# Performance work log

Hardware: AMD Instinct MI355X
Metric: run time of the kernel (lower is better)

The kernel has to match this reference:

```python
import jax, jax.numpy as jnp
import numpy as np
import math

B, S, D = 4, 2048, 1024

def setup_inputs() -> dict:
    key = jax.random.key(0)
    k_x, k_q, k_k, k_v = jax.random.split(key, 4)
    scale = 1.0 / math.sqrt(D)
    return {
        "x": jax.random.normal(k_x, (B, S, D), dtype=jnp.float32),
        "W_Q": jax.random.normal(k_q, (D, D), dtype=jnp.float32) * scale,
        "W_K": jax.random.normal(k_k, (D, D), dtype=jnp.float32) * scale,
        "W_V": jax.random.normal(k_v, (D, D), dtype=jnp.float32) * scale,
    }

def reference(x, W_Q, W_K, W_V):
    # nn.Linear(bias=False): y = x @ W.T
    Q = jnp.einsum('bsd,ed->bse', x, W_Q)
    K = jnp.einsum('bsd,ed->bse', x, W_K)
    V = jnp.einsum('bsd,ed->bse', x, W_V)
    scores = jnp.einsum('bqd,bkd->bqk', Q, K) / jnp.sqrt(jnp.asarray(Q.shape[-1], Q.dtype))
    weight = jax.nn.softmax(scores, axis=-1)  # [B,S,S]
    return jnp.einsum('bqk,bkd->bqd', weight, V)
```

## Files before the change

kernel.cpp:

```cpp
#include <hip/hip_runtime.h>
#include <stdint.h>

typedef __bf16 bf16;
typedef __bf16 bf16x8 __attribute__((ext_vector_type(8)));
typedef __bf16 bf16x4 __attribute__((ext_vector_type(4)));
typedef float f32x4 __attribute__((ext_vector_type(4)));

__device__ inline void gload_lds16(const void* g, void* l) {
  __builtin_amdgcn_global_load_lds(
      (__attribute__((address_space(1))) void*)g,
      (__attribute__((address_space(3))) void*)l, 16, 0, 0);
}

__global__ __launch_bounds__(256) void cvt_f32_bf16(const float* __restrict__ in,
                                                    bf16* __restrict__ out, int n4) {
  int i = blockIdx.x * blockDim.x + threadIdx.x;
  int stride = gridDim.x * blockDim.x;
  for (; i < n4; i += stride) {
    float4 v = ((const float4*)in)[i];
    bf16x4 o;
    o[0] = (bf16)v.x; o[1] = (bf16)v.y; o[2] = (bf16)v.z; o[3] = (bf16)v.w;
    ((bf16x4*)out)[i] = o;
  }
}

template <int MODE, int BN>
__global__ __launch_bounds__(512, 2) void gemm8(
    const bf16* __restrict__ Ag, const bf16* __restrict__ Bg,
    void* __restrict__ Cg, void* __restrict__ C2g,
    long lda, long ldb, long ldc,
    long sA, long sB, long sC, int K, float scale)
{
  constexpr int BUFSZ = 32768 + BN * 128;
  constexpr int MACC = (BN == 256) ? 8 : 4;
  __shared__ alignas(16) char lds[2 * BUFSZ];
  const int tid = threadIdx.x;
  const int l = tid & 63;
  const int wv = tid >> 6;
  const int fr = l & 15;
  const int kch = l >> 4;
  const int m0 = blockIdx.y * 256;
  const int n0 = blockIdx.x * BN;
  const bf16* Ab = Ag + (long)blockIdx.z * sA;
  const bf16* Bb = Bg + (long)blockIdx.z * sB;

  const int wm = (BN == 256) ? (wv >> 2) : (wv >> 1);
  const int wn = (BN == 256) ? (wv & 3) : (wv & 1);

  int a_rd, b_rd;
  if constexpr (BN == 256) {
    a_rd = fr * 128 + (((wm * 4 + kch) ^ (fr & 7)) << 4);
    b_rd = (wn & 1) * 8192 + fr * 128 + ((((wn >> 1) * 4 + kch) ^ (fr & 7)) << 4);
  } else {
    a_rd = (wm & 1) * 8192 + fr * 128 + ((((wm >> 1) * 4 + kch) ^ (fr & 7)) << 4);
    b_rd = fr * 128 + (((wn * 4 + kch) ^ (fr & 7)) << 4);
  }

  const int se = (tid & 7) ^ ((tid >> 3) & 7);
  const int s_rowA = (se >> 2) * 128 + (tid >> 3);
  const int s_rowB = (BN == 256) ? s_rowA : ((se >> 2) * 64 + (tid >> 3));
  const int s_k = (se & 3) * 8;
  const int wb16 = (tid & 448) * 16;

  const int NT = K >> 6;
  f32x4 acc[MACC][4] = {};

  auto stageA = [&](int tile, int kh, int buf) {
#pragma unroll
    for (int rd = 0; rd < 2; ++rd)
      gload_lds16(Ab + (long)(m0 + s_rowA + rd * 64) * lda + tile * 64 + kh * 32 + s_k,
                  lds + buf * BUFSZ + kh * 16384 + rd * 8192 + wb16);
  };
  auto stageB = [&](int tile, int kh, int buf) {
    if constexpr (BN == 256) {
#pragma unroll
      for (int rd = 0; rd < 2; ++rd)
        gload_lds16(Bb + (long)(n0 + s_rowB + rd * 64) * ldb + tile * 64 + kh * 32 + s_k,
                    lds + buf * BUFSZ + 32768 + kh * 16384 + rd * 8192 + wb16);
    } else {
      gload_lds16(Bb + (long)(n0 + s_rowB) * ldb + tile * 64 + kh * 32 + s_k,
                  lds + buf * BUFSZ + 32768 + kh * 8192 + wb16);
    }
  };

  stageA(0, 0, 0); stageB(0, 0, 0); stageA(0, 1, 0); stageB(0, 1, 0);
  stageA(min(1, NT - 1), 0, 1); stageB(min(1, NT - 1), 0, 1);
  if constexpr (BN == 256) asm volatile("s_waitcnt vmcnt(4)" ::: "memory");
  else                     asm volatile("s_waitcnt vmcnt(3)" ::: "memory");
  __builtin_amdgcn_sched_barrier(0);
  __builtin_amdgcn_s_barrier();

  for (int t = 0; t < NT; ++t) {
    const char* bufA = lds + (t & 1) * BUFSZ;
    const char* bufB = bufA + 32768;
    const int t1 = min(t + 1, NT - 1);
    const int t2 = min(t + 2, NT - 1);
    const int nb = (t & 1) ^ 1;
    const int cur = t & 1;

    if constexpr (BN == 256) {
      bf16x8 bfg[4], af[4];
      stageA(t1, 1, nb);
#pragma unroll
      for (int n = 0; n < 4; ++n) bfg[n] = *(const bf16x8*)(bufB + n * 2048 + b_rd);
#pragma unroll
      for (int m = 0; m < 4; ++m) af[m] = *(const bf16x8*)(bufA + m * 2048 + a_rd);
      __builtin_amdgcn_s_barrier();
      __builtin_amdgcn_s_setprio(1);
#pragma unroll
      for (int m = 0; m < 4; ++m)
#pragma unroll
        for (int n = 0; n < 4; ++n)
          acc[m][n] = __builtin_amdgcn_mfma_f32_16x16x32_bf16(af[m], bfg[n], acc[m][n], 0, 0, 0);
      __builtin_amdgcn_s_setprio(0);
      __builtin_amdgcn_s_barrier();
      stageB(t1, 1, nb);
#pragma unroll
      for (int m = 0; m < 4; ++m) af[m] = *(const bf16x8*)(bufA + 8192 + m * 2048 + a_rd);
      __builtin_amdgcn_s_barrier();
      __builtin_amdgcn_s_setprio(1);
#pragma unroll
      for (int m = 0; m < 4; ++m)
#pragma unroll
        for (int n = 0; n < 4; ++n)
          acc[4 + m][n] = __builtin_amdgcn_mfma_f32_16x16x32_bf16(af[m], bfg[n], acc[4 + m][n], 0, 0, 0);
      __builtin_amdgcn_s_setprio(0);
      __builtin_amdgcn_s_barrier();
      stageA(t2, 0, cur);
#pragma unroll
      for (int n = 0; n < 4; ++n) bfg[n] = *(const bf16x8*)(bufB + 16384 + n * 2048 + b_rd);
#pragma unroll
      for (int m = 0; m < 4; ++m) af[m] = *(const bf16x8*)(bufA + 16384 + m * 2048 + a_rd);
      __builtin_amdgcn_s_barrier();
      __builtin_amdgcn_s_setprio(1);
#pragma unroll
      for (int m = 0; m < 4; ++m)
#pragma unroll
        for (int n = 0; n < 4; ++n)
          acc[m][n] = __builtin_amdgcn_mfma_f32_16x16x32_bf16(af[m], bfg[n], acc[m][n], 0, 0, 0);
      __builtin_amdgcn_s_setprio(0);
      __builtin_amdgcn_s_barrier();
      stageB(t2, 0, cur);
#pragma unroll
      for (int m = 0; m < 4; ++m) af[m] = *(const bf16x8*)(bufA + 16384 + 8192 + m * 2048 + a_rd);
      __builtin_amdgcn_s_barrier();
      __builtin_amdgcn_s_setprio(1);
#pragma unroll
      for (int m = 0; m < 4; ++m)
#pragma unroll
        for (int n = 0; n < 4; ++n)
          acc[4 + m][n] = __builtin_amdgcn_mfma_f32_16x16x32_bf16(af[m], bfg[n], acc[4 + m][n], 0, 0, 0);
      __builtin_amdgcn_s_setprio(0);
      asm volatile("s_waitcnt vmcnt(4)" ::: "memory");
      __builtin_amdgcn_sched_barrier(0);
      __builtin_amdgcn_s_barrier();
    } else {
      bf16x8 bfg[4], af[4];
      stageA(t1, 1, nb); stageB(t1, 1, nb);
#pragma unroll
      for (int n = 0; n < 4; ++n) bfg[n] = *(const bf16x8*)(bufB + n * 2048 + b_rd);
#pragma unroll
      for (int m = 0; m < 4; ++m) af[m] = *(const bf16x8*)(bufA + m * 2048 + a_rd);
      __builtin_amdgcn_s_barrier();
      __builtin_amdgcn_s_setprio(1);
#pragma unroll
      for (int m = 0; m < 4; ++m)
#pragma unroll
        for (int n = 0; n < 4; ++n)
          acc[m][n] = __builtin_amdgcn_mfma_f32_16x16x32_bf16(af[m], bfg[n], acc[m][n], 0, 0, 0);
      __builtin_amdgcn_s_setprio(0);
      __builtin_amdgcn_s_barrier();
      stageA(t2, 0, cur); stageB(t2, 0, cur);
#pragma unroll
      for (int n = 0; n < 4; ++n) bfg[n] = *(const bf16x8*)(bufB + 8192 + n * 2048 + b_rd);
#pragma unroll
      for (int m = 0; m < 4; ++m) af[m] = *(const bf16x8*)(bufA + 16384 + m * 2048 + a_rd);
      __builtin_amdgcn_s_barrier();
      __builtin_amdgcn_s_setprio(1);
#pragma unroll
      for (int m = 0; m < 4; ++m)
#pragma unroll
        for (int n = 0; n < 4; ++n)
          acc[m][n] = __builtin_amdgcn_mfma_f32_16x16x32_bf16(af[m], bfg[n], acc[m][n], 0, 0, 0);
      __builtin_amdgcn_s_setprio(0);
      asm volatile("s_waitcnt vmcnt(3)" ::: "memory");
      __builtin_amdgcn_sched_barrier(0);
      __builtin_amdgcn_s_barrier();
    }
  }
  asm volatile("s_waitcnt vmcnt(0)" ::: "memory");

#pragma unroll
  for (int mf = 0; mf < MACC; ++mf) {
    int row;
    if constexpr (BN == 256)
      row = m0 + wm * 128 + (mf >> 2) * 64 + (mf & 3) * 16 + (l >> 4) * 4;
    else
      row = m0 + wm * 64 + mf * 16 + (l >> 4) * 4;
#pragma unroll
    for (int n = 0; n < 4; ++n) {
      const int col = n0 + wn * 64 + n * 16 + fr;
      if constexpr (MODE == 0) {
        if (col < 2048) {
          bf16* C = (bf16*)Cg;
#pragma unroll
          for (int r = 0; r < 4; ++r)
            C[(long)(row + r) * 2048 + col] = (bf16)acc[mf][n][r];
        } else {
          bf16* Vt = (bf16*)C2g;
          const int d = col - 2048;
          const int b = row >> 11;
          const int s = row & 2047;
          bf16x4 pk;
#pragma unroll
          for (int r = 0; r < 4; ++r) pk[r] = (bf16)acc[mf][n][r];
          *(bf16x4*)(Vt + (long)b * 2097152 + (long)d * 2048 + s) = pk;
        }
      } else if constexpr (MODE == 1) {
        float* C = (float*)Cg + (long)blockIdx.z * sC;
#pragma unroll
        for (int r = 0; r < 4; ++r)
          C[(long)(row + r) * ldc + col] = acc[mf][n][r] * scale;
      } else {
        bf16* C = (bf16*)Cg + (long)blockIdx.z * sC;
#pragma unroll
        for (int r = 0; r < 4; ++r)
          C[(long)(row + r) * ldc + col] = (bf16)(acc[mf][n][r] * scale);
      }
    }
  }
}

__global__ __launch_bounds__(256) void softmax_k(const bf16* __restrict__ Sm,
                                                 bf16* __restrict__ P, int cols) {
  __shared__ float red[8];
  const long row = blockIdx.x;
  const bf16* sr = Sm + row * (long)cols;
  bf16* pr = P + row * (long)cols;
  const int t = threadIdx.x;
  bf16x8 v = *(const bf16x8*)(sr + t * 8);
  float e[8];
#pragma unroll
  for (int j = 0; j < 8; ++j) e[j] = (float)v[j];
  float m = e[0];
#pragma unroll
  for (int j = 1; j < 8; ++j) m = fmaxf(m, e[j]);
#pragma unroll
  for (int o = 32; o; o >>= 1) m = fmaxf(m, __shfl_xor(m, o));
  if ((t & 63) == 0) red[t >> 6] = m;
  __syncthreads();
  m = fmaxf(fmaxf(red[0], red[1]), fmaxf(red[2], red[3]));
  float s = 0.f;
#pragma unroll
  for (int j = 0; j < 8; ++j) { e[j] = __expf(e[j] - m); s += e[j]; }
#pragma unroll
  for (int o = 32; o; o >>= 1) s += __shfl_xor(s, o);
  if ((t & 63) == 0) red[4 + (t >> 6)] = s;
  __syncthreads();
  s = red[4] + red[5] + red[6] + red[7];
  const float inv = 1.0f / s;
  bf16x8 o8;
#pragma unroll
  for (int j = 0; j < 8; ++j) o8[j] = (bf16)(e[j] * inv);
  *(bf16x8*)(pr + t * 8) = o8;
}

extern "C" void kernel_launch(void* const* d_in, const int* in_sizes, int n_in,
                              void* d_out, int out_size, void* d_ws, size_t ws_size,
                              hipStream_t stream) {
  const float* x  = (const float*)d_in[0];
  const float* Wq = (const float*)d_in[1];
  const float* Wk = (const float*)d_in[2];
  const float* Wv = (const float*)d_in[3];
  float* out = (float*)d_out;

  const int D = 1024;

  char* ws = (char*)d_ws;
  bf16* QKbuf = (bf16*)(ws);
  bf16* P     = (bf16*)(ws);
  bf16* Vt    = (bf16*)(ws + 33554432);
  bf16* scb   = (bf16*)(ws + 50331648);
  bf16* xb    = (bf16*)(ws + 50331648);
  bf16* Wb    = (bf16*)(ws + 67108864);

  dim3 b256(256, 1, 1), b512(512, 1, 1);

  cvt_f32_bf16<<<2048, b256, 0, stream>>>(x, xb, 8192 * 1024 / 4);
  cvt_f32_bf16<<<512, b256, 0, stream>>>(Wq, Wb,             D * D / 4);
  cvt_f32_bf16<<<512, b256, 0, stream>>>(Wk, Wb + 1048576,   D * D / 4);
  cvt_f32_bf16<<<512, b256, 0, stream>>>(Wv, Wb + 2097152,   D * D / 4);

  gemm8<0, 128><<<dim3(24, 32, 1), b512, 0, stream>>>(
      xb, Wb, QKbuf, Vt, 1024, 1024, 2048, 0, 0, 0, 1024, 1.f);

  gemm8<2, 256><<<dim3(8, 8, 4), b512, 0, stream>>>(
      QKbuf, QKbuf + 1024, scb, nullptr, 2048, 2048, 2048,
      4194304, 4194304, 4194304, 1024, 0.03125f);

  softmax_k<<<8192, b256, 0, stream>>>(scb, P, 2048);

  gemm8<1, 128><<<dim3(8, 8, 4), b512, 0, stream>>>(
      P, Vt, out, nullptr, 2048, 2048, 1024,
      4194304, 2097152, 2097152, 2048, 1.f);
}
```

Before: 183.7 us.

## Fuse conversion kernels and use 128x128 GEMM tiles for projection and PV

The four f32-to-bf16 conversion launches become one combined kernel, which cuts launch overhead. A new 256-thread GEMM with 128x128 tiles replaces the 256x128 512-thread variant for the QKV projection and the P·V product. This doubles the grid size (1536 and 512 blocks) for better CU occupancy and load balance on the 256-CU device, at the cost of lower per-block data reuse. The 256x256 gemm8 is kept only for the QK^T scores.

```diff
diff --git a/kernel.cpp b/kernel.cpp
--- a/kernel.cpp
+++ b/kernel.cpp
@@ -12,27 +12,37 @@
       (__attribute__((address_space(3))) void*)l, 16, 0, 0);
 }
 
-__global__ __launch_bounds__(256) void cvt_f32_bf16(const float* __restrict__ in,
-                                                    bf16* __restrict__ out, int n4) {
-  int i = blockIdx.x * blockDim.x + threadIdx.x;
-  int stride = gridDim.x * blockDim.x;
-  for (; i < n4; i += stride) {
-    float4 v = ((const float4*)in)[i];
+__global__ __launch_bounds__(256) void cvt_all(
+    const float* __restrict__ x, const float* __restrict__ wq,
+    const float* __restrict__ wk, const float* __restrict__ wv,
+    bf16* __restrict__ xb, bf16* __restrict__ Wb) {
+  const int NX = 2097152;
+  const int NW = 262144;
+  int i = blockIdx.x * 256 + threadIdx.x;
+  const int stride = gridDim.x * 256;
+  for (int p = i; p < NX + 3 * NW; p += stride) {
+    const float* src; bf16* dst; int off;
+    if (p < NX) { src = x; dst = xb; off = p; }
+    else {
+      int q = p - NX; int w = q >> 18; off = q & (NW - 1);
+      src = (w == 0) ? wq : ((w == 1) ? wk : wv);
+      dst = Wb + (long)w * 1048576;
+    }
+    float4 v = ((const float4*)src)[off];
     bf16x4 o;
     o[0] = (bf16)v.x; o[1] = (bf16)v.y; o[2] = (bf16)v.z; o[3] = (bf16)v.w;
-    ((bf16x4*)out)[i] = o;
-  }
-}
-
-template <int MODE, int BN>
+    ((bf16x4*)dst)[off] = o;
+  }
+}
+
+template <int MODE>
 __global__ __launch_bounds__(512, 2) void gemm8(
     const bf16* __restrict__ Ag, const bf16* __restrict__ Bg,
-    void* __restrict__ Cg, void* __restrict__ C2g,
+    void* __restrict__ Cg,
     long lda, long ldb, long ldc,
     long sA, long sB, long sC, int K, float scale)
 {
-  constexpr int BUFSZ = 32768 + BN * 128;
-  constexpr int MACC = (BN == 256) ? 8 : 4;
+  constexpr int BUFSZ = 65536;
   __shared__ alignas(16) char lds[2 * BUFSZ];
   const int tid = threadIdx.x;
   const int l = tid & 63;
@@ -40,53 +50,40 @@
   const int fr = l & 15;
   const int kch = l >> 4;
   const int m0 = blockIdx.y * 256;
-  const int n0 = blockIdx.x * BN;
+  const int n0 = blockIdx.x * 256;
   const bf16* Ab = Ag + (long)blockIdx.z * sA;
   const bf16* Bb = Bg + (long)blockIdx.z * sB;
 
-  const int wm = (BN == 256) ? (wv >> 2) : (wv >> 1);
-  const int wn = (BN == 256) ? (wv & 3) : (wv & 1);
-
-  int a_rd, b_rd;
-  if constexpr (BN == 256) {
-    a_rd = fr * 128 + (((wm * 4 + kch) ^ (fr & 7)) << 4);
-    b_rd = (wn & 1) * 8192 + fr * 128 + ((((wn >> 1) * 4 + kch) ^ (fr & 7)) << 4);
-  } else {
-    a_rd = (wm & 1) * 8192 + fr * 128 + ((((wm >> 1) * 4 + kch) ^ (fr & 7)) << 4);
-    b_rd = fr * 128 + (((wn * 4 + kch) ^ (fr & 7)) << 4);
-  }
+  const int wm = wv >> 2;
+  const int wn = wv & 3;
+
+  const int a_rd = fr * 128 + (((wm * 4 + kch) ^ (fr & 7)) << 4);
+  const int b_rd = (wn & 1) * 8192 + fr * 128 + ((((wn >> 1) * 4 + kch) ^ (fr & 7)) << 4);
 
   const int se = (tid & 7) ^ ((tid >> 3) & 7);
-  const int s_rowA = (se >> 2) * 128 + (tid >> 3);
-  const int s_rowB = (BN == 256) ? s_rowA : ((se >> 2) * 64 + (tid >> 3));
+  const int s_row = (se >> 2) * 128 + (tid >> 3);
   const int s_k = (se & 3) * 8;
   const int wb16 = (tid & 448) * 16;
 
   const int NT = K >> 6;
-  f32x4 acc[MACC][4] = {};
+  f32x4 acc[8][4] = {};
 
   auto stageA = [&](int tile, int kh, int buf) {
 #pragma unroll
     for (int rd = 0; rd < 2; ++rd)
-      gload_lds16(Ab + (long)(m0 + s_rowA + rd * 64) * lda + tile * 64 + kh * 32 + s_k,
+      gload_lds16(Ab + (long)(m0 + s_row + rd * 64) * lda + tile * 64 + kh * 32 + s_k,
                   lds + buf * BUFSZ + kh * 16384 + rd * 8192 + wb16);
   };
   auto stageB = [&](int tile, int kh, int buf) {
-    if constexpr (BN == 256) {
-#pragma unroll
-      for (int rd = 0; rd < 2; ++rd)
-        gload_lds16(Bb + (long)(n0 + s_rowB + rd * 64) * ldb + tile * 64 + kh * 32 + s_k,
-                    lds + buf * BUFSZ + 32768 + kh * 16384 + rd * 8192 + wb16);
-    } else {
-      gload_lds16(Bb + (long)(n0 + s_rowB) * ldb + tile * 64 + kh * 32 + s_k,
-                  lds + buf * BUFSZ + 32768 + kh * 8192 + wb16);
-    }
+#pragma unroll
+    for (int rd = 0; rd < 2; ++rd)
+      gload_lds16(Bb + (long)(n0 + s_row + rd * 64) * ldb + tile * 64 + kh * 32 + s_k,
+                  lds + buf * BUFSZ + 32768 + kh * 16384 + rd * 8192 + wb16);
   };
 
   stageA(0, 0, 0); stageB(0, 0, 0); stageA(0, 1, 0); stageB(0, 1, 0);
   stageA(min(1, NT - 1), 0, 1); stageB(min(1, NT - 1), 0, 1);
-  if constexpr (BN == 256) asm volatile("s_waitcnt vmcnt(4)" ::: "memory");
-  else                     asm volatile("s_waitcnt vmcnt(3)" ::: "memory");
+  asm volatile("s_waitcnt vmcnt(4)" ::: "memory");
   __builtin_amdgcn_sched_barrier(0);
   __builtin_amdgcn_s_barrier();
 
@@ -98,105 +95,173 @@
     const int nb = (t & 1) ^ 1;
     const int cur = t & 1;
 
-    if constexpr (BN == 256) {
-      bf16x8 bfg[4], af[4];
-      stageA(t1, 1, nb);
-#pragma unroll
-      for (int n = 0; n < 4; ++n) bfg[n] = *(const bf16x8*)(bufB + n * 2048 + b_rd);
-#pragma unroll
-      for (int m = 0; m < 4; ++m) af[m] = *(const bf16x8*)(bufA + m * 2048 + a_rd);
-      __builtin_amdgcn_s_barrier();
-      __builtin_amdgcn_s_setprio(1);
-#pragma unroll
-      for (int m = 0; m < 4; ++m)
-#pragma unroll
-        for (int n = 0; n < 4; ++n)
-          acc[m][n] = __builtin_amdgcn_mfma_f32_16x16x32_bf16(af[m], bfg[n], acc[m][n], 0, 0, 0);
-      __builtin_amdgcn_s_setprio(0);
-      __builtin_amdgcn_s_barrier();
-      stageB(t1, 1, nb);
-#pragma unroll
-      for (int m = 0; m < 4; ++m) af[m] = *(const bf16x8*)(bufA + 8192 + m * 2048 + a_rd);
-      __builtin_amdgcn_s_barrier();
-      __builtin_amdgcn_s_setprio(1);
-#pragma unroll
-      for (int m = 0; m < 4; ++m)
-#pragma unroll
-        for (int n = 0; n < 4; ++n)
-          acc[4 + m][n] = __builtin_amdgcn_mfma_f32_16x16x32_bf16(af[m], bfg[n], acc[4 + m][n], 0, 0, 0);
-      __builtin_amdgcn_s_setprio(0);
-      __builtin_amdgcn_s_barrier();
-      stageA(t2, 0, cur);
-#pragma unroll
-      for (int n = 0; n < 4; ++n) bfg[n] = *(const bf16x8*)(bufB + 16384 + n * 2048 + b_rd);
-#pragma unroll
-      for (int m = 0; m < 4; ++m) af[m] = *(const bf16x8*)(bufA + 16384 + m * 2048 + a_rd);
-      __builtin_amdgcn_s_barrier();
-      __builtin_amdgcn_s_setprio(1);
-#pragma unroll
-      for (int m = 0; m < 4; ++m)
-#pragma unroll
-        for (int n = 0; n < 4; ++n)
-          acc[m][n] = __builtin_amdgcn_mfma_f32_16x16x32_bf16(af[m], bfg[n], acc[m][n], 0, 0, 0);
-      __builtin_amdgcn_s_setprio(0);
-      __builtin_amdgcn_s_barrier();
-      stageB(t2, 0, cur);
-#pragma unroll
-      for (int m = 0; m < 4; ++m) af[m] = *(const bf16x8*)(bufA + 16384 + 8192 + m * 2048 + a_rd);
-      __builtin_amdgcn_s_barrier();
-      __builtin_amdgcn_s_setprio(1);
-#pragma unroll
-      for (int m = 0; m < 4; ++m)
-#pragma unroll
-        for (int n = 0; n < 4; ++n)
-          acc[4 + m][n] = __builtin_amdgcn_mfma_f32_16x16x32_bf16(af[m], bfg[n], acc[4 + m][n], 0, 0, 0);
-      __builtin_amdgcn_s_setprio(0);
-      asm volatile("s_waitcnt vmcnt(4)" ::: "memory");
-      __builtin_amdgcn_sched_barrier(0);
-      __builtin_amdgcn_s_barrier();
-    } else {
-      bf16x8 bfg[4], af[4];
-      stageA(t1, 1, nb); stageB(t1, 1, nb);
-#pragma unroll
-      for (int n = 0; n < 4; ++n) bfg[n] = *(const bf16x8*)(bufB + n * 2048 + b_rd);
-#pragma unroll
-      for (int m = 0; m < 4; ++m) af[m] = *(const bf16x8*)(bufA + m * 2048 + a_rd);
-      __builtin_amdgcn_s_barrier();
-      __builtin_amdgcn_s_setprio(1);
-#pragma unroll
-      for (int m = 0; m < 4; ++m)
-#pragma unroll
-        for (int n = 0; n < 4; ++n)
-          acc[m][n] = __builtin_amdgcn_mfma_f32_16x16x32_bf16(af[m], bfg[n], acc[m][n], 0, 0, 0);
-      __builtin_amdgcn_s_setprio(0);
-      __builtin_amdgcn_s_barrier();
-      stageA(t2, 0, cur); stageB(t2, 0, cur);
-#pragma unroll
-      for (int n = 0; n < 4; ++n) bfg[n] = *(const bf16x8*)(bufB + 8192 + n * 2048 + b_rd);
-#pragma unroll
-      for (int m = 0; m < 4; ++m) af[m] = *(const bf16x8*)(bufA + 16384 + m * 2048 + a_rd);
-      __builtin_amdgcn_s_barrier();
-      __builtin_amdgcn_s_setprio(1);
-#pragma unroll
-      for (int m = 0; m < 4; ++m)
-#pragma unroll
-        for (int n = 0; n < 4; ++n)
-          acc[m][n] = __builtin_amdgcn_mfma_f32_16x16x32_bf16(af[m], bfg[n], acc[m][n], 0, 0, 0);
-      __builtin_amdgcn_s_setprio(0);
-      asm volatile("s_waitcnt vmcnt(3)" ::: "memory");
-      __builtin_amdgcn_sched_barrier(0);
-      __builtin_amdgcn_s_barrier();
+    bf16x8 bfg[4], af[4];
+    stageA(t1, 1, nb);
+#pragma unroll
+    for (int n = 0; n < 4; ++n) bfg[n] = *(const bf16x8*)(bufB + n * 2048 + b_rd);
+#pragma unroll
+    for (int m = 0; m < 4; ++m) af[m] = *(const bf16x8*)(bufA + m * 2048 + a_rd);
+    __builtin_amdgcn_s_barrier();
+    __builtin_amdgcn_s_setprio(1);
+#pragma unroll
+    for (int m = 0; m < 4; ++m)
+#pragma unroll
+      for (int n = 0; n < 4; ++n)
+        acc[m][n] = __builtin_amdgcn_mfma_f32_16x16x32_bf16(af[m], bfg[n], acc[m][n], 0, 0, 0);
+    __builtin_amdgcn_s_setprio(0);
+    __builtin_amdgcn_s_barrier();
+    stageB(t1, 1, nb);
+#pragma unroll
+    for (int m = 0; m < 4; ++m) af[m] = *(const bf16x8*)(bufA + 8192 + m * 2048 + a_rd);
+    __builtin_amdgcn_s_barrier();
+    __builtin_amdgcn_s_setprio(1);
+#pragma unroll
+    for (int m = 0; m < 4; ++m)
+#pragma unroll
+      for (int n = 0; n < 4; ++n)
+        acc[4 + m][n] = __builtin_amdgcn_mfma_f32_16x16x32_bf16(af[m], bfg[n], acc[4 + m][n], 0, 0, 0);
+    __builtin_amdgcn_s_setprio(0);
+    __builtin_amdgcn_s_barrier();
+    stageA(t2, 0, cur);
+#pragma unroll
+    for (int n = 0; n < 4; ++n) bfg[n] = *(const bf16x8*)(bufB + 16384 + n * 2048 + b_rd);
+#pragma unroll
+    for (int m = 0; m < 4; ++m) af[m] = *(const bf16x8*)(bufA + 16384 + m * 2048 + a_rd);
+    __builtin_amdgcn_s_barrier();
+    __builtin_amdgcn_s_setprio(1);
+#pragma unroll
+    for (int m = 0; m < 4; ++m)
+#pragma unroll
+      for (int n = 0; n < 4; ++n)
+        acc[m][n] = __builtin_amdgcn_mfma_f32_16x16x32_bf16(af[m], bfg[n], acc[m][n], 0, 0, 0);
+    __builtin_amdgcn_s_setprio(0);
+    __builtin_amdgcn_s_barrier();
+    stageB(t2, 0, cur);
+#pragma unroll
+    for (int m = 0; m < 4; ++m) af[m] = *(const bf16x8*)(bufA + 16384 + 8192 + m * 2048 + a_rd);
+    __builtin_amdgcn_s_barrier();
+    __builtin_amdgcn_s_setprio(1);
+#pragma unroll
+    for (int m = 0; m < 4; ++m)
+#pragma unroll
+      for (int n = 0; n < 4; ++n)
+        acc[4 + m][n] = __builtin_amdgcn_mfma_f32_16x16x32_bf16(af[m], bfg[n], acc[4 + m][n], 0, 0, 0);
+    __builtin_amdgcn_s_setprio(0);
+    asm volatile("s_waitcnt vmcnt(4)" ::: "memory");
+    __builtin_amdgcn_sched_barrier(0);
+    __builtin_amdgcn_s_barrier();
+  }
+  asm volatile("s_waitcnt vmcnt(0)" ::: "memory");
+
+#pragma unroll
+  for (int mf = 0; mf < 8; ++mf) {
+    const int row = m0 + wm * 128 + (mf >> 2) * 64 + (mf & 3) * 16 + (l >> 4) * 4;
+#pragma unroll
+    for (int n = 0; n < 4; ++n) {
+      const int col = n0 + wn * 64 + n * 16 + fr;
+      bf16* C = (bf16*)Cg + (long)blockIdx.z * sC;
+#pragma unroll
+      for (int r = 0; r < 4; ++r)
+        C[(long)(row + r) * ldc + col] = (bf16)(acc[mf][n][r] * scale);
     }
   }
+}
+
+template <int MODE>
+__global__ __launch_bounds__(256, 2) void gemm2h(
+    const bf16* __restrict__ Ag, const bf16* __restrict__ Bg,
+    void* __restrict__ Cg, void* __restrict__ C2g,
+    long lda, long ldb, long ldc,
+    long sA, long sB, long sC, int K, float scale)
+{
+  constexpr int BUFSZ = 32768;
+  __shared__ alignas(16) char lds[2 * BUFSZ];
+  const int tid = threadIdx.x;
+  const int l = tid & 63;
+  const int wv = tid >> 6;
+  const int wm = wv >> 1, wn = wv & 1;
+  const int fr = l & 15;
+  const int kch = l >> 4;
+  const int m0 = blockIdx.y * 128;
+  const int n0 = blockIdx.x * 128;
+  const bf16* Ab = Ag + (long)blockIdx.z * sA;
+  const bf16* Bb = Bg + (long)blockIdx.z * sB;
+
+  const int a_rd = fr * 128 + (((wm * 4 + kch) ^ (fr & 7)) << 4);
+  const int b_rd = fr * 128 + (((wn * 4 + kch) ^ (fr & 7)) << 4);
+
+  const int se = (tid & 7) ^ ((tid >> 3) & 7);
+  const int s_row = (se >> 2) * 64 + (tid >> 3);
+  const int s_k = (se & 3) * 8;
+  const int wb16 = (tid >> 6) * 1024;
+
+  const int NT = K >> 6;
+  f32x4 acc[4][4] = {};
+
+  auto stageA = [&](int tile, int kh, int buf) {
+#pragma unroll
+    for (int rd = 0; rd < 2; ++rd)
+      gload_lds16(Ab + (long)(m0 + s_row + rd * 32) * lda + tile * 64 + kh * 32 + s_k,
+                  lds + buf * BUFSZ + kh * 8192 + rd * 4096 + wb16);
+  };
+  auto stageB = [&](int tile, int kh, int buf) {
+#pragma unroll
+    for (int rd = 0; rd < 2; ++rd)
+      gload_lds16(Bb + (long)(n0 + s_row + rd * 32) * ldb + tile * 64 + kh * 32 + s_k,
+                  lds + buf * BUFSZ + 16384 + kh * 8192 + rd * 4096 + wb16);
+  };
+
+  stageA(0, 0, 0); stageB(0, 0, 0); stageA(0, 1, 0); stageB(0, 1, 0);
+  stageA(min(1, NT - 1), 0, 1); stageB(min(1, NT - 1), 0, 1);
+  asm volatile("s_waitcnt vmcnt(4)" ::: "memory");
+  __builtin_amdgcn_sched_barrier(0);
+  __builtin_amdgcn_s_barrier();
+
+  for (int t = 0; t < NT; ++t) {
+    const char* bufA = lds + (t & 1) * BUFSZ;
+    const char* bufB = bufA + 16384;
+    const int t1 = min(t + 1, NT - 1);
+    const int t2 = min(t + 2, NT - 1);
+    const int nb = (t & 1) ^ 1;
+    const int cur = t & 1;
+
+    bf16x8 bfg[4], af[4];
+    stageA(t1, 1, nb); stageB(t1, 1, nb);
+#pragma unroll
+    for (int n = 0; n < 4; ++n) bfg[n] = *(const bf16x8*)(bufB + n * 2048 + b_rd);
+#pragma unroll
+    for (int m = 0; m < 4; ++m) af[m] = *(const bf16x8*)(bufA + m * 2048 + a_rd);
+    __builtin_amdgcn_s_barrier();
+    __builtin_amdgcn_s_setprio(1);
+#pragma unroll
+    for (int m = 0; m < 4; ++m)
+#pragma unroll
+      for (int n = 0; n < 4; ++n)
+        acc[m][n] = __builtin_amdgcn_mfma_f32_16x16x32_bf16(af[m], bfg[n], acc[m][n], 0, 0, 0);
+    __builtin_amdgcn_s_setprio(0);
+    __builtin_amdgcn_s_barrier();
+    stageA(t2, 0, cur); stageB(t2, 0, cur);
+#pragma unroll
+    for (int n = 0; n < 4; ++n) bfg[n] = *(const bf16x8*)(bufB + 8192 + n * 2048 + b_rd);
+#pragma unroll
+    for (int m = 0; m < 4; ++m) af[m] = *(const bf16x8*)(bufA + 8192 + m * 2048 + a_rd);
+    __builtin_amdgcn_s_barrier();
+    __builtin_amdgcn_s_setprio(1);
+#pragma unroll
+    for (int m = 0; m < 4; ++m)
+#pragma unroll
+      for (int n = 0; n < 4; ++n)
+        acc[m][n] = __builtin_amdgcn_mfma_f32_16x16x32_bf16(af[m], bfg[n], acc[m][n], 0, 0, 0);
+    __builtin_amdgcn_s_setprio(0);
+    asm volatile("s_waitcnt vmcnt(4)" ::: "memory");
+    __builtin_amdgcn_sched_barrier(0);
+    __builtin_amdgcn_s_barrier();
+  }
   asm volatile("s_waitcnt vmcnt(0)" ::: "memory");
 
 #pragma unroll
-  for (int mf = 0; mf < MACC; ++mf) {
-    int row;
-    if constexpr (BN == 256)
-      row = m0 + wm * 128 + (mf >> 2) * 64 + (mf & 3) * 16 + (l >> 4) * 4;
-    else
-      row = m0 + wm * 64 + mf * 16 + (l >> 4) * 4;
+  for (int mf = 0; mf < 4; ++mf) {
+    const int row = m0 + wm * 64 + mf * 16 + (l >> 4) * 4;
 #pragma unroll
     for (int n = 0; n < 4; ++n) {
       const int col = n0 + wn * 64 + n * 16 + fr;
@@ -216,16 +281,11 @@
           for (int r = 0; r < 4; ++r) pk[r] = (bf16)acc[mf][n][r];
           *(bf16x4*)(Vt + (long)b * 2097152 + (long)d * 2048 + s) = pk;
         }
-      } else if constexpr (MODE == 1) {
+      } else {
         float* C = (float*)Cg + (long)blockIdx.z * sC;
 #pragma unroll
         for (int r = 0; r < 4; ++r)
           C[(long)(row + r) * ldc + col] = acc[mf][n][r] * scale;
-      } else {
-        bf16* C = (bf16*)Cg + (long)blockIdx.z * sC;
-#pragma unroll
-        for (int r = 0; r < 4; ++r)
-          C[(long)(row + r) * ldc + col] = (bf16)(acc[mf][n][r] * scale);
       }
     }
   }
@@ -274,8 +334,6 @@
   const float* Wv = (const float*)d_in[3];
   float* out = (float*)d_out;
 
-  const int D = 1024;
-
   char* ws = (char*)d_ws;
   bf16* QKbuf = (bf16*)(ws);
   bf16* P     = (bf16*)(ws);
@@ -286,21 +344,18 @@
 
   dim3 b256(256, 1, 1), b512(512, 1, 1);
 
-  cvt_f32_bf16<<<2048, b256, 0, stream>>>(x, xb, 8192 * 1024 / 4);
-  cvt_f32_bf16<<<512, b256, 0, stream>>>(Wq, Wb,             D * D / 4);
-  cvt_f32_bf16<<<512, b256, 0, stream>>>(Wk, Wb + 1048576,   D * D / 4);
-  cvt_f32_bf16<<<512, b256, 0, stream>>>(Wv, Wb + 2097152,   D * D / 4);
-
-  gemm8<0, 128><<<dim3(24, 32, 1), b512, 0, stream>>>(
+  cvt_all<<<2048, b256, 0, stream>>>(x, Wq, Wk, Wv, xb, Wb);
+
+  gemm2h<0><<<dim3(24, 64, 1), b256, 0, stream>>>(
       xb, Wb, QKbuf, Vt, 1024, 1024, 2048, 0, 0, 0, 1024, 1.f);
 
-  gemm8<2, 256><<<dim3(8, 8, 4), b512, 0, stream>>>(
-      QKbuf, QKbuf + 1024, scb, nullptr, 2048, 2048, 2048,
+  gemm8<2><<<dim3(8, 8, 4), b512, 0, stream>>>(
+      QKbuf, QKbuf + 1024, scb, 2048, 2048, 2048,
       4194304, 4194304, 4194304, 1024, 0.03125f);
 
   softmax_k<<<8192, b256, 0, stream>>>(scb, P, 2048);
 
-  gemm8<1, 128><<<dim3(8, 8, 4), b512, 0, stream>>>(
+  gemm2h<1><<<dim3(8, 16, 4), b256, 0, stream>>>(
       P, Vt, out, nullptr, 2048, 2048, 1024,
       4194304, 2097152, 2097152, 2048, 1.f);
 }
```

Result: no change. 183.9 us (+0.1%).
